# Kernel optimization log

Measured on AMD Instinct MI355X. Metric: run time of the kernel, lower is better.

## Reference

```python
import jax, jax.numpy as jnp
import numpy as np

V = 6890   # SMPL vertices
K = 24     # joints
NB = 10    # shape betas
NP = 207   # pose blendshape basis = 23*9
PARENTS = np.array([-1, 0, 0, 0, 1, 2, 3, 4, 5, 6, 7, 8, 9, 9, 9, 12, 13, 14, 16, 17, 18, 19, 20, 21])


def setup_inputs() -> dict:
    key = jax.random.key(0)
    ks = jax.random.split(key, 8)
    B = 1024
    body_pose = jax.random.normal(ks[0], (B, 69), dtype=jnp.float32) * 0.2
    betas = jax.random.normal(ks[1], (B, NB), dtype=jnp.float32)
    global_orient = jax.random.normal(ks[2], (B, 3), dtype=jnp.float32) * 0.2
    v_template = jax.random.normal(ks[3], (V, 3), dtype=jnp.float32) * 0.1
    shapedirs = jax.random.normal(ks[4], (V, 3, NB), dtype=jnp.float32) * 0.01
    posedirs = jax.random.normal(ks[5], (NP, V * 3), dtype=jnp.float32) * 0.01
    J_regressor = jax.nn.softmax(jax.random.normal(ks[6], (K, V), dtype=jnp.float32), axis=-1)
    lbs_weights = jax.nn.softmax(jax.random.normal(ks[7], (V, K), dtype=jnp.float32) * 4.0, axis=-1)
    parents = jnp.asarray(PARENTS, dtype=jnp.int32)
    return dict(body_pose=body_pose, betas=betas, global_orient=global_orient,
                v_template=v_template, shapedirs=shapedirs, posedirs=posedirs,
                J_regressor=J_regressor, lbs_weights=lbs_weights, parents=parents)


def _rodrigues(aa):
    # aa: [..., 3] axis-angle -> [..., 3, 3] rotation matrices
    angle = jnp.linalg.norm(aa + 1e-8, axis=-1, keepdims=True)  # [...,1]
    axis = aa / angle
    sin = jnp.sin(angle)[..., None]
    cos = jnp.cos(angle)[..., None]
    rx, ry, rz = axis[..., 0], axis[..., 1], axis[..., 2]
    z = jnp.zeros_like(rx)
    Km = jnp.stack([z, -rz, ry, rz, z, -rx, -ry, rx, z], axis=-1).reshape(aa.shape[:-1] + (3, 3))
    ident = jnp.eye(3, dtype=aa.dtype)
    return ident + sin * Km + (1.0 - cos) * (Km @ Km)


def reference(body_pose, betas, global_orient, v_template, shapedirs, posedirs,
              J_regressor, lbs_weights, parents):
    full_pose = jnp.concatenate([global_orient, body_pose], axis=1)  # [B,72]
    B = betas.shape[0]
    dtype = betas.dtype

    # shape blend shapes
    v_shaped = v_template + jnp.einsum('bl,vkl->bvk', betas, shapedirs)  # [B,V,3]
    # rest joints
    joints_t = jnp.einsum('jv,bvk->bjk', J_regressor, v_shaped)          # [B,K,3]

    # pose -> rotation matrices (pose2rot=True path)
    rot_mats = _rodrigues(full_pose.reshape(B, K, 3))                    # [B,K,3,3]

    # pose blend shapes
    ident = jnp.eye(3, dtype=dtype)
    pose_feature = (rot_mats[:, 1:] - ident).reshape(B, NP)              # [B,207]
    v_posed = v_shaped + (pose_feature @ posedirs).reshape(B, V, 3)

    # kinematic chain (batch_rigid_transform)
    rel_joints = joints_t.at[:, 1:].add(-joints_t[:, PARENTS[1:]])       # [B,K,3]
    tm = jnp.concatenate([rot_mats, rel_joints[..., None]], axis=-1)     # [B,K,3,4]
    bottom = jnp.broadcast_to(jnp.array([0., 0., 0., 1.], dtype=dtype), (B, K, 1, 4))
    tm = jnp.concatenate([tm, bottom], axis=-2)                          # [B,K,4,4]
    chain = [tm[:, 0]]
    for i in range(1, K):  # fixed small kinematic tree
        chain.append(chain[PARENTS[i]] @ tm[:, i])
    transforms = jnp.stack(chain, axis=1)                                # [B,K,4,4]
    joints = transforms[..., :3, 3]                                      # posed joints

    # relative transforms: subtract rotated rest-joint position
    A = transforms.at[..., :3, 3].add(
        -jnp.einsum('bkij,bkj->bki', transforms[..., :3, :3], joints_t))  # [B,K,4,4]

    # linear blend skinning
    T = jnp.einsum('vk,bkij->bvij', lbs_weights, A)                      # [B,V,4,4]
    vertices = jnp.einsum('bvij,bvj->bvi', T[..., :3, :3], v_posed) + T[..., :3, 3]
    return vertices, joints_t, joints, rot_mats
```

## Files before the change

kernel.cpp:

```cpp
#include <hip/hip_runtime.h>
#include <hip/hip_bf16.h>

#define VNUM 6890
#define KJ 24
#define NBETA 10
#define NPOSE 207
#define KPAD 224
#define BATCH 1024
#define N3 20670
#define N3PAD 20672
#define VPAD 6912

#define OUT_V  0
#define OUT_JT 21166080
#define OUT_J  21239808
#define OUT_RM 21313536

#define WS_JVJS 0
#define WS_ABF  792
#define WS_WBF  246552
#define WS_PFB  384792
#define WS_PDT  499480

typedef unsigned short ushort;
typedef __attribute__((ext_vector_type(8))) short short8v;
typedef __attribute__((ext_vector_type(4))) float floatx4;

__device__ __forceinline__ ushort f2bfu(float x) {
  __hip_bfloat16 h = __float2bfloat16(x);
  union { __hip_bfloat16 h; ushort u; } cv; cv.h = h; return cv.u;
}

__global__ __launch_bounds__(256) void jreg_kernel(
    const float* __restrict__ Jr, const float* __restrict__ vt,
    const float* __restrict__ sd, float* __restrict__ JvJs) {
  const int j = blockIdx.x;
  const int chunk = blockIdx.y;
  const int t = threadIdx.x;
  const int lane = t & 63, wid = t >> 6;
  const int vbeg = chunk * 1723;
  const int vend = (vbeg + 1723 < VNUM) ? vbeg + 1723 : VNUM;
  __shared__ float red[4][33];
  float acc[33];
#pragma unroll
  for (int q = 0; q < 33; q++) acc[q] = 0.0f;
  for (int v = vbeg + t; v < vend; v += 256) {
    float r = Jr[j * VNUM + v];
    const float* vtp = vt + v * 3;
    const float* sdp = sd + v * 30;
    acc[0] += r * vtp[0];
    acc[1] += r * vtp[1];
    acc[2] += r * vtp[2];
#pragma unroll
    for (int q = 0; q < 30; q++) acc[3 + q] += r * sdp[q];
  }
#pragma unroll
  for (int q = 0; q < 33; q++) {
    float x = acc[q];
    for (int off = 32; off > 0; off >>= 1) x += __shfl_down(x, off, 64);
    if (lane == 0) red[wid][q] = x;
  }
  __syncthreads();
  if (t < 33)
    atomicAdd(&JvJs[j * 33 + t], red[0][t] + red[1][t] + red[2][t] + red[3][t]);
}

__global__ __launch_bounds__(64) void batch_prep(
    const float* __restrict__ body_pose, const float* __restrict__ betas,
    const float* __restrict__ global_orient, const float* __restrict__ JvJs,
    float* __restrict__ out_jt, float* __restrict__ out_j, float* __restrict__ out_rm,
    ushort* __restrict__ pfb, ushort* __restrict__ Abf) {
  const int b = blockIdx.x;
  const int t = threadIdx.x;
  __shared__ float R[24][9];
  __shared__ float jt[24][3];
  __shared__ float chR[24][9];
  __shared__ float cht[24][3];

  if (t < 24) {
    float ax, ay, az;
    if (t == 0) {
      ax = global_orient[b * 3 + 0];
      ay = global_orient[b * 3 + 1];
      az = global_orient[b * 3 + 2];
    } else {
      const float* p = body_pose + (size_t)b * 69 + (t - 1) * 3;
      ax = p[0]; ay = p[1]; az = p[2];
    }
    float px = ax + 1e-8f, py = ay + 1e-8f, pz = az + 1e-8f;
    float angle = sqrtf(px * px + py * py + pz * pz);
    float inv = 1.0f / angle;
    float rx = ax * inv, ry = ay * inv, rz = az * inv;
    float s = sinf(angle), c = cosf(angle);
    float cc = 1.0f - c;
    float m[9];
    m[0] = 1.0f - cc * (ry * ry + rz * rz);
    m[1] = -s * rz + cc * rx * ry;
    m[2] =  s * ry + cc * rx * rz;
    m[3] =  s * rz + cc * rx * ry;
    m[4] = 1.0f - cc * (rx * rx + rz * rz);
    m[5] = -s * rx + cc * ry * rz;
    m[6] = -s * ry + cc * rx * rz;
    m[7] =  s * rx + cc * ry * rz;
    m[8] = 1.0f - cc * (rx * rx + ry * ry);
#pragma unroll
    for (int e = 0; e < 9; e++) {
      R[t][e] = m[e];
      out_rm[(size_t)b * 216 + t * 9 + e] = m[e];
    }
  }
  for (int idx = t; idx < 72; idx += 64) {
    int j = idx / 3, c = idx % 3;
    const float* JJ = JvJs + j * 33;
    float s = JJ[c];
    const float* be = betas + (size_t)b * NBETA;
#pragma unroll
    for (int l = 0; l < NBETA; l++) s += be[l] * JJ[3 + c * 10 + l];
    jt[j][c] = s;
    out_jt[(size_t)b * 72 + idx] = s;
  }
  __syncthreads();
  for (int mI = t; mI < KPAD; mI += 64) {
    float val = 0.0f;
    if (mI < NPOSE) {
      int k = 1 + mI / 9, e = mI % 9;
      val = R[k][e] - ((e == 0 || e == 4 || e == 8) ? 1.0f : 0.0f);
    } else if (mI < NPOSE + NBETA) {
      val = betas[(size_t)b * NBETA + (mI - NPOSE)];
    }
    pfb[(size_t)b * KPAD + mI] = f2bfu(val);
  }
  if (t == 0) {
    const int par[24] = {-1, 0, 0, 0, 1, 2, 3, 4, 5, 6, 7, 8, 9, 9, 9, 12, 13, 14, 16, 17, 18, 19, 20, 21};
#pragma unroll
    for (int e = 0; e < 9; e++) chR[0][e] = R[0][e];
    cht[0][0] = jt[0][0]; cht[0][1] = jt[0][1]; cht[0][2] = jt[0][2];
    for (int k = 1; k < 24; k++) {
      int p = par[k];
      float rel0 = jt[k][0] - jt[p][0];
      float rel1 = jt[k][1] - jt[p][1];
      float rel2 = jt[k][2] - jt[p][2];
#pragma unroll
      for (int i = 0; i < 3; i++) {
        float a0 = chR[p][i * 3 + 0], a1 = chR[p][i * 3 + 1], a2 = chR[p][i * 3 + 2];
        chR[k][i * 3 + 0] = a0 * R[k][0] + a1 * R[k][3] + a2 * R[k][6];
        chR[k][i * 3 + 1] = a0 * R[k][1] + a1 * R[k][4] + a2 * R[k][7];
        chR[k][i * 3 + 2] = a0 * R[k][2] + a1 * R[k][5] + a2 * R[k][8];
        cht[k][i] = a0 * rel0 + a1 * rel1 + a2 * rel2 + cht[p][i];
      }
    }
  }
  __syncthreads();
  if (t < 24) {
    int k = t;
#pragma unroll
    for (int i = 0; i < 3; i++) out_j[(size_t)b * 72 + k * 3 + i] = cht[k][i];
  }
  for (int e = t; e < 480; e += 64) {
    int n = e / 40, k = e - (e / 40) * 40;
    float val = 0.0f;
    if (k < 24) {
      int i = n >> 2, jj = n & 3;
      if (jj < 3) {
        val = chR[k][i * 3 + jj];
      } else {
        val = cht[k][i] - (chR[k][i * 3 + 0] * jt[k][0] +
                           chR[k][i * 3 + 1] * jt[k][1] +
                           chR[k][i * 3 + 2] * jt[k][2]);
      }
    }
    Abf[(size_t)b * 480 + e] = f2bfu(val);
  }
}

__global__ __launch_bounds__(256) void transpose_pd(
    const float* __restrict__ pd, ushort* __restrict__ pdT,
    const float* __restrict__ sd,
    const float* __restrict__ w, ushort* __restrict__ wbf) {
  {
    int lb = blockIdx.y * 323 + blockIdx.x;
    if (lb < 1080) {
      int i = lb * 256 + threadIdx.x;
      int v = i / 40, k = i - v * 40;
      float x = (v < VNUM && k < 24) ? w[v * 24 + k] : 0.0f;
      wbf[i] = f2bfu(x);
    }
  }
  __shared__ float tile[32][65];
  const int t = threadIdx.x;
  const int n0 = blockIdx.x * 64;
  const int k0 = blockIdx.y * 32;
  const int c = t & 63;
  for (int r = t >> 6; r < 32; r += 4) {
    int k = k0 + r, n = n0 + c;
    float x = 0.0f;
    if (n < N3) {
      if (k < NPOSE) x = pd[(size_t)k * N3 + n];
      else if (k < NPOSE + NBETA) x = sd[(size_t)n * 10 + (k - NPOSE)];
    }
    tile[r][c] = x;
  }
  __syncthreads();
  const int n = t >> 2;
  const int j0 = (t & 3) * 8;
  unsigned int outw[4];
#pragma unroll
  for (int jj = 0; jj < 4; jj++) {
    unsigned int lo = f2bfu(tile[j0 + jj * 2][n]);
    unsigned int hi = f2bfu(tile[j0 + jj * 2 + 1][n]);
    outw[jj] = lo | (hi << 16);
  }
  *(uint4*)&pdT[(size_t)(n0 + n) * KPAD + k0 + j0] =
      make_uint4(outw[0], outw[1], outw[2], outw[3]);
}

__global__ __launch_bounds__(256, 5) void vposed_mfma(
    const ushort* __restrict__ pfb, const ushort* __restrict__ pdT,
    const float* __restrict__ vt, float* __restrict__ vposed) {
  __shared__ __align__(16) ushort Bs[64 * KPAD];
  __shared__ float vtS[64];
  const int tid = threadIdx.x;
  const int lane = tid & 63, w = tid >> 6;
  const int l15 = lane & 15, quad = lane >> 4;
  const int bm = blockIdx.x * 64;
  const int bn = blockIdx.y * 64;
  const int mrow = w * 16 + l15;

  short8v av[7];
  const ushort* arow = pfb + (size_t)(bm + mrow) * KPAD;
#pragma unroll
  for (int kb = 0; kb < 7; kb++)
    av[kb] = *(const short8v*)(arow + kb * 32 + quad * 8);

  {
    const uint4* srcB = (const uint4*)(pdT + (size_t)bn * KPAD);
    uint4* dB = (uint4*)Bs;
#pragma unroll
    for (int r = 0; r < 7; r++) dB[tid + r * 256] = srcB[tid + r * 256];
    if (tid < 64) vtS[tid] = (bn + tid < N3) ? vt[bn + tid] : 0.0f;
  }
  __syncthreads();

  floatx4 acc[4];
  const floatx4 zero = {0.0f, 0.0f, 0.0f, 0.0f};
#pragma unroll
  for (int ns = 0; ns < 4; ns++) acc[ns] = zero;

#pragma unroll
  for (int kb = 0; kb < 7; kb++) {
#pragma unroll
    for (int ns = 0; ns < 4; ns++) {
      short8v bv = *(const short8v*)&Bs[(ns * 16 + l15) * KPAD + kb * 32 + quad * 8];
      acc[ns] = __builtin_amdgcn_mfma_f32_16x16x32_bf16(av[kb], bv, acc[ns], 0, 0, 0);
    }
  }

#pragma unroll
  for (int ns = 0; ns < 4; ns++) {
    int nl = ns * 16 + l15;
    int gn = bn + nl;
    if (gn < N3) {
      float vtv = vtS[nl];
#pragma unroll
      for (int reg = 0; reg < 4; reg++) {
        int ml = w * 16 + quad * 4 + reg;
        vposed[(size_t)(bm + ml) * N3 + gn] = acc[ns][reg] + vtv;
      }
    }
  }
}

__global__ __launch_bounds__(256) void blend_mfma(
    const ushort* __restrict__ wbf, const ushort* __restrict__ Abf,
    float* __restrict__ out_v) {
  __shared__ __align__(16) ushort Ws[64 * 40];
  __shared__ __align__(16) ushort Bs[16 * 480 + 160];
  const int tid = threadIdx.x;
  const int lane = tid & 63, wv = tid >> 6;
  const int quad = lane >> 4, l15 = lane & 15;
  const int v0 = blockIdx.x * 64;
  const int b0 = blockIdx.y * 16;

  {
    const uint4* srcW = (const uint4*)(wbf + (size_t)v0 * 40);
    uint4* dstW = (uint4*)Ws;
    dstW[tid] = srcW[tid];
    if (tid < 64) dstW[256 + tid] = srcW[256 + tid];
    const uint4* srcB = (const uint4*)(Abf + (size_t)b0 * 480);
    uint4* dstB = (uint4*)Bs;
#pragma unroll
    for (int r = 0; r < 3; r++) dstB[tid + r * 256] = srcB[tid + r * 256];
    if (tid < 192) dstB[768 + tid] = srcB[768 + tid];
    if (tid < 20) dstB[960 + tid] = make_uint4(0u, 0u, 0u, 0u);
  }
  __syncthreads();

  const short8v wf = *(const short8v*)&Ws[(wv * 16 + l15) * 40 + quad * 8];

  const int gv = v0 + wv * 16 + l15;
  const bool active = (quad < 3) && (gv < VNUM);
  const size_t vbase = (size_t)gv * 3;

  float px[4], py[4], pz[4];
#pragma unroll
  for (int i = 0; i < 4; i++) {
    if (active) {
      const float* p = out_v + (size_t)(b0 + i) * N3 + vbase;
      px[i] = p[0]; py[i] = p[1]; pz[i] = p[2];
    }
  }

#pragma unroll
  for (int b = 0; b < 16; b++) {
    const int slot = b & 3;
    short8v afrag = *(const short8v*)&Bs[b * 480 + l15 * 40 + quad * 8];
    floatx4 acc = {0.0f, 0.0f, 0.0f, 0.0f};
    acc = __builtin_amdgcn_mfma_f32_16x16x32_bf16(afrag, wf, acc, 0, 0, 0);
    if (active) {
      out_v[(size_t)(b0 + b) * N3 + vbase + quad] =
          acc[0] * px[slot] + acc[1] * py[slot] + acc[2] * pz[slot] + acc[3];
      if (b < 12) {
        const float* p = out_v + (size_t)(b0 + b + 4) * N3 + vbase;
        px[slot] = p[0]; py[slot] = p[1]; pz[slot] = p[2];
      }
    }
  }
}

extern "C" void kernel_launch(void* const* d_in, const int* in_sizes, int n_in,
                              void* d_out, int out_size, void* d_ws, size_t ws_size,
                              hipStream_t stream) {
  const float* body_pose     = (const float*)d_in[0];
  const float* betas         = (const float*)d_in[1];
  const float* global_orient = (const float*)d_in[2];
  const float* v_template    = (const float*)d_in[3];
  const float* shapedirs     = (const float*)d_in[4];
  const float* posedirs      = (const float*)d_in[5];
  const float* J_regressor   = (const float*)d_in[6];
  const float* lbs_weights   = (const float*)d_in[7];

  float* out = (float*)d_out;
  float* out_v  = out + OUT_V;
  float* out_jt = out + OUT_JT;
  float* out_j  = out + OUT_J;
  float* out_rm = out + OUT_RM;

  float* ws = (float*)d_ws;
  float* JvJs = ws + WS_JVJS;
  ushort* Abf = (ushort*)(ws + WS_ABF);
  ushort* wbf = (ushort*)(ws + WS_WBF);
  ushort* pfb = (ushort*)(ws + WS_PFB);
  ushort* pdT = (ushort*)(ws + WS_PDT);

  hipMemsetAsync(JvJs, 0, KJ * 33 * sizeof(float), stream);
  jreg_kernel<<<dim3(KJ, 4), 256, 0, stream>>>(J_regressor, v_template, shapedirs, JvJs);
  transpose_pd<<<dim3(323, 7), 256, 0, stream>>>(posedirs, pdT, shapedirs,
                                                 lbs_weights, wbf);
  batch_prep<<<BATCH, 64, 0, stream>>>(body_pose, betas, global_orient, JvJs,
                                       out_jt, out_j, out_rm, pfb, Abf);
  vposed_mfma<<<dim3(16, 323), 256, 0, stream>>>(pfb, pdT, v_template, out_v);
  blend_mfma<<<dim3(108, 64), 256, 0, stream>>>(wbf, Abf, out_v);
}
```

Measured before the change: 212.6 us.

## Fuse pose-blend GEMM and skinning into one kernel with LDS staging

Merges the v_posed MFMA GEMM and the linear blend skinning kernel into a single kernel. Each block computes posed vertices for 16 vertices by 64 batches, stages them in shared memory and then applies the per-vertex blended transforms. This removes the full write and read-back of the intermediate posed-vertex array in global memory. In exchange it uses a narrower GEMM tile with more redundant loads of pdT and pfb across blocks. It also relies on a wave-local waitcnt instead of a block barrier between the two phases.

```diff
diff --git a/kernel.cpp b/kernel.cpp
--- a/kernel.cpp
+++ b/kernel.cpp
@@ -214,115 +214,83 @@
       make_uint4(outw[0], outw[1], outw[2], outw[3]);
 }
 
-__global__ __launch_bounds__(256, 5) void vposed_mfma(
+__global__ __launch_bounds__(256, 4) void fused_mfma(
     const ushort* __restrict__ pfb, const ushort* __restrict__ pdT,
-    const float* __restrict__ vt, float* __restrict__ vposed) {
-  __shared__ __align__(16) ushort Bs[64 * KPAD];
-  __shared__ float vtS[64];
+    const float* __restrict__ vt, const ushort* __restrict__ wbf,
+    const ushort* __restrict__ Abf, float* __restrict__ out_v) {
+  __shared__ __align__(16) ushort Bs[48 * KPAD];
+  __shared__ float vpS[64 * 50];
+  __shared__ float vtS[48];
   const int tid = threadIdx.x;
-  const int lane = tid & 63, w = tid >> 6;
+  const int lane = tid & 63, wv = tid >> 6;
   const int l15 = lane & 15, quad = lane >> 4;
-  const int bm = blockIdx.x * 64;
-  const int bn = blockIdx.y * 64;
-  const int mrow = w * 16 + l15;
+  const int v0 = blockIdx.x * 16;
+  const int bm = blockIdx.y * 64;
+
+  const short8v wf = *(const short8v*)(wbf + (size_t)(v0 + l15) * 40 + quad * 8);
 
   short8v av[7];
-  const ushort* arow = pfb + (size_t)(bm + mrow) * KPAD;
+  const ushort* arow = pfb + (size_t)(bm + wv * 16 + l15) * KPAD;
 #pragma unroll
   for (int kb = 0; kb < 7; kb++)
     av[kb] = *(const short8v*)(arow + kb * 32 + quad * 8);
 
   {
-    const uint4* srcB = (const uint4*)(pdT + (size_t)bn * KPAD);
+    const uint4* src = (const uint4*)pdT;
     uint4* dB = (uint4*)Bs;
-#pragma unroll
-    for (int r = 0; r < 7; r++) dB[tid + r * 256] = srcB[tid + r * 256];
-    if (tid < 64) vtS[tid] = (bn + tid < N3) ? vt[bn + tid] : 0.0f;
-  }
-  __syncthreads();
-
-  floatx4 acc[4];
+    for (int e = tid; e < 48 * 28; e += 256) {
+      int row = e / 28, q = e - row * 28;
+      int n = v0 * 3 + row;
+      if (n >= N3PAD) n = 0;
+      dB[row * 28 + q] = src[(size_t)n * 28 + q];
+    }
+    if (tid < 48) {
+      int gn = v0 * 3 + tid;
+      vtS[tid] = (gn < N3) ? vt[gn] : 0.0f;
+    }
+  }
+  __syncthreads();
+
+  floatx4 acc[3];
   const floatx4 zero = {0.0f, 0.0f, 0.0f, 0.0f};
 #pragma unroll
-  for (int ns = 0; ns < 4; ns++) acc[ns] = zero;
-
+  for (int ns = 0; ns < 3; ns++) acc[ns] = zero;
 #pragma unroll
   for (int kb = 0; kb < 7; kb++) {
 #pragma unroll
-    for (int ns = 0; ns < 4; ns++) {
+    for (int ns = 0; ns < 3; ns++) {
       short8v bv = *(const short8v*)&Bs[(ns * 16 + l15) * KPAD + kb * 32 + quad * 8];
       acc[ns] = __builtin_amdgcn_mfma_f32_16x16x32_bf16(av[kb], bv, acc[ns], 0, 0, 0);
     }
   }
-
-#pragma unroll
-  for (int ns = 0; ns < 4; ns++) {
-    int nl = ns * 16 + l15;
-    int gn = bn + nl;
-    if (gn < N3) {
-      float vtv = vtS[nl];
-#pragma unroll
-      for (int reg = 0; reg < 4; reg++) {
-        int ml = w * 16 + quad * 4 + reg;
-        vposed[(size_t)(bm + ml) * N3 + gn] = acc[ns][reg] + vtv;
-      }
-    }
-  }
-}
-
-__global__ __launch_bounds__(256) void blend_mfma(
-    const ushort* __restrict__ wbf, const ushort* __restrict__ Abf,
-    float* __restrict__ out_v) {
-  __shared__ __align__(16) ushort Ws[64 * 40];
-  __shared__ __align__(16) ushort Bs[16 * 480 + 160];
-  const int tid = threadIdx.x;
-  const int lane = tid & 63, wv = tid >> 6;
-  const int quad = lane >> 4, l15 = lane & 15;
-  const int v0 = blockIdx.x * 64;
-  const int b0 = blockIdx.y * 16;
-
-  {
-    const uint4* srcW = (const uint4*)(wbf + (size_t)v0 * 40);
-    uint4* dstW = (uint4*)Ws;
-    dstW[tid] = srcW[tid];
-    if (tid < 64) dstW[256 + tid] = srcW[256 + tid];
-    const uint4* srcB = (const uint4*)(Abf + (size_t)b0 * 480);
-    uint4* dstB = (uint4*)Bs;
-#pragma unroll
-    for (int r = 0; r < 3; r++) dstB[tid + r * 256] = srcB[tid + r * 256];
-    if (tid < 192) dstB[768 + tid] = srcB[768 + tid];
-    if (tid < 20) dstB[960 + tid] = make_uint4(0u, 0u, 0u, 0u);
-  }
-  __syncthreads();
-
-  const short8v wf = *(const short8v*)&Ws[(wv * 16 + l15) * 40 + quad * 8];
-
-  const int gv = v0 + wv * 16 + l15;
+#pragma unroll
+  for (int ns = 0; ns < 3; ns++) {
+    int col = ns * 16 + l15;
+    float vtv = vtS[col];
+#pragma unroll
+    for (int r = 0; r < 4; r++)
+      vpS[(wv * 16 + quad * 4 + r) * 50 + col] = acc[ns][r] + vtv;
+  }
+  __builtin_amdgcn_sched_barrier(0);
+  __builtin_amdgcn_s_waitcnt(0xc07f);
+  __builtin_amdgcn_sched_barrier(0);
+
+  const int gv = v0 + l15;
   const bool active = (quad < 3) && (gv < VNUM);
   const size_t vbase = (size_t)gv * 3;
 
-  float px[4], py[4], pz[4];
-#pragma unroll
-  for (int i = 0; i < 4; i++) {
+#pragma unroll
+  for (int i = 0; i < 16; i++) {
+    const int b = wv * 16 + i;
+    const size_t gb = (size_t)(bm + b);
+    short8v afrag = *(const short8v*)(Abf + gb * 480 + l15 * 40 + quad * 8);
+    floatx4 t = zero;
+    t = __builtin_amdgcn_mfma_f32_16x16x32_bf16(afrag, wf, t, 0, 0, 0);
+    float px = vpS[b * 50 + 3 * l15 + 0];
+    float py = vpS[b * 50 + 3 * l15 + 1];
+    float pz = vpS[b * 50 + 3 * l15 + 2];
     if (active) {
-      const float* p = out_v + (size_t)(b0 + i) * N3 + vbase;
-      px[i] = p[0]; py[i] = p[1]; pz[i] = p[2];
-    }
-  }
-
-#pragma unroll
-  for (int b = 0; b < 16; b++) {
-    const int slot = b & 3;
-    short8v afrag = *(const short8v*)&Bs[b * 480 + l15 * 40 + quad * 8];
-    floatx4 acc = {0.0f, 0.0f, 0.0f, 0.0f};
-    acc = __builtin_amdgcn_mfma_f32_16x16x32_bf16(afrag, wf, acc, 0, 0, 0);
-    if (active) {
-      out_v[(size_t)(b0 + b) * N3 + vbase + quad] =
-          acc[0] * px[slot] + acc[1] * py[slot] + acc[2] * pz[slot] + acc[3];
-      if (b < 12) {
-        const float* p = out_v + (size_t)(b0 + b + 4) * N3 + vbase;
-        px[slot] = p[0]; py[slot] = p[1]; pz[slot] = p[2];
-      }
+      out_v[gb * N3 + vbase + quad] = t[0] * px + t[1] * py + t[2] * pz + t[3];
     }
   }
 }
@@ -358,6 +326,6 @@
                                                  lbs_weights, wbf);
   batch_prep<<<BATCH, 64, 0, stream>>>(body_pose, betas, global_orient, JvJs,
                                        out_jt, out_j, out_rm, pfb, Abf);
-  vposed_mfma<<<dim3(16, 323), 256, 0, stream>>>(pfb, pdT, v_template, out_v);
-  blend_mfma<<<dim3(108, 64), 256, 0, stream>>>(wbf, Abf, out_v);
-}
+  fused_mfma<<<dim3(431, 16), 256, 0, stream>>>(pfb, pdT, v_template, wbf,
+                                                Abf, out_v);
+}
```

New measurement: 220.9 us. 3.9% more time.
